# Optimization experiments

Hardware: AMD Instinct MI355X
Metric: run time of the kernel (lower is better)

Reference implementation:

```python
import jax, jax.numpy as jnp
import numpy as np

DIM = 128
CODEBOOK_SIZE = 1024

def setup_inputs() -> dict:
    key = jax.random.key(0)
    k1, k2 = jax.random.split(key)
    x = jax.random.normal(k1, (16, 4096, DIM), dtype=jnp.float32)
    embed = jax.random.normal(k2, (CODEBOOK_SIZE, DIM), dtype=jnp.float32)
    return {"x": x, "embed": embed}

def reference(x, embed):
    # preprocess: flatten leading dims -> (N, d)
    shape = x.shape
    flat = x.reshape(-1, shape[-1])  # (N, d)
    x_sq = jnp.sum(flat * flat, axis=1, keepdims=True)        # (N, 1)
    e_sq = jnp.sum(embed * embed, axis=1)[None, :]            # (1, K)
    dist = -(x_sq - 2.0 * (flat @ embed.T) + e_sq)            # (N, K)
    embed_ind = jnp.argmax(dist, axis=-1)                     # (N,)
    embed_ind = embed_ind.reshape(shape[:-1])                 # (...,)
    quantize = jnp.take(embed, embed_ind, axis=0)             # (..., d)
    return (quantize, embed_ind)
```

## Files before the change

### kernel.cpp

```cpp
#include <hip/hip_runtime.h>

#define NRD   65536
#define DIMD  128
#define KCB   1024
#define RPB   64
#define NBLK  (NRD / RPB)
#define MARGIN 0.10f

typedef float f32x4 __attribute__((ext_vector_type(4)));
typedef _Float16 half8 __attribute__((ext_vector_type(8)));

#define WS_ESQ   0
#define WS_CNT   4096
#define WS_LIST  8192
#define WS_B     270336
#define WS_ET2   532480
#define WS_NEED  1056768

__device__ inline half8 pack_h(float4 a, float4 b) {
    half8 r;
    r[0]=(_Float16)a.x; r[1]=(_Float16)a.y; r[2]=(_Float16)a.z; r[3]=(_Float16)a.w;
    r[4]=(_Float16)b.x; r[5]=(_Float16)b.y; r[6]=(_Float16)b.z; r[7]=(_Float16)b.w;
    return r;
}

__global__ __launch_bounds__(256, 2) void prep_kernel(const float* __restrict__ embed,
                                                      float* __restrict__ esq,
                                                      float4* __restrict__ bblob,
                                                      float4* __restrict__ et4,
                                                      int* __restrict__ cnt,
                                                      int doTrans) {
    __shared__ float tile[64][129];
    const int t = threadIdx.x;
    {
        int gw   = blockIdx.x * 4 + (t >> 6);
        int lane = t & 63;
        const float* row = embed + (size_t)gw * DIMD;
        float a = row[lane], b = row[lane + 64];
        float v = a * a + b * b;
        #pragma unroll
        for (int off = 32; off >= 1; off >>= 1) v += __shfl_xor(v, off, 64);
        if (lane == 0) esq[gw] = v;
    }
    if (blockIdx.x < 64) {
        int tid  = blockIdx.x * 256 + t;
        int lane = tid & 63;
        int ctg  = (tid >> 6) & 15;
        int ksh  = (tid >> 10) & 1;
        int s    = tid >> 11;
        int chunk = s >> 1, kh = s & 1;
        int ks = kh * 2 + ksh;
        int l15 = lane & 15, l4 = lane >> 4;
        int code = chunk * 256 + ctg * 16 + l15;
        int d0   = ks * 32 + l4 * 8;
        const float4* e4 = (const float4*)(embed + (size_t)code * DIMD + d0);
        half8 v = pack_h(e4[0], e4[1]);
        bblob[tid] = *(float4*)&v;
    }
    if (doTrans && blockIdx.x >= 64 && blockIdx.x < 80) {
        const int c0 = (blockIdx.x - 64) * 64;
        #pragma unroll
        for (int i = 0; i < 8; ++i) {
            int u = t + i * 256;
            int row = u >> 5, col4 = u & 31;
            float4 v = ((const float4*)embed)[(size_t)(c0 + row) * 32 + col4];
            tile[row][col4 * 4 + 0] = v.x;
            tile[row][col4 * 4 + 1] = v.y;
            tile[row][col4 * 4 + 2] = v.z;
            tile[row][col4 * 4 + 3] = v.w;
        }
        __syncthreads();
        #pragma unroll
        for (int i = 0; i < 8; ++i) {
            int u = t + i * 256;
            int d = u >> 4, off = u & 15;
            float4 v;
            v.x = tile[off * 4 + 0][d];
            v.y = tile[off * 4 + 1][d];
            v.z = tile[off * 4 + 2][d];
            v.w = tile[off * 4 + 3][d];
            et4[(size_t)d * 256 + (c0 >> 2) + off] = v;
        }
    }
    if (blockIdx.x == 128 && t == 0) cnt[0] = 0;
}

__global__ __launch_bounds__(512, 4) void vq_mfma(const float* __restrict__ x,
                                                  const float* __restrict__ embed,
                                                  const float* __restrict__ esq,
                                                  const float4* __restrict__ bblob,
                                                  float* __restrict__ out_q,
                                                  float* __restrict__ out_idx,
                                                  int* __restrict__ cnt,
                                                  int* __restrict__ list) {
    __shared__ __align__(16) short Bb[32][512];
    __shared__ float rbest[4][RPB];
    __shared__ int   rmeta[4][RPB];
    __shared__ float rb2[4][RPB];

    const int t    = threadIdx.x;
    const int lane = t & 63;
    const int w    = __builtin_amdgcn_readfirstlane(t >> 6);
    const int rg   = w >> 2, cg = w & 3;
    const int l15  = lane & 15, l4 = lane >> 4;
    const int row0 = blockIdx.x * RPB;

    short (*Atrans)[4][512] = (short (*)[4][512])&Bb[0][0];

    const int ksA = w & 3, jh = w >> 2;
    const float4* xs = (const float4*)(x + (size_t)(row0 + lane) * DIMD + ksA * 32 + jh * 16);
    float4 xv0 = xs[0], xv1 = xs[1], xv2 = xs[2], xv3 = xs[3];

    const int rtA = lane >> 4, riA = lane & 15;
    *(half8*)&Atrans[ksA][rtA][((jh * 2 + 0) * 16 + riA) * 8] = pack_h(xv0, xv1);
    *(half8*)&Atrans[ksA][rtA][((jh * 2 + 1) * 16 + riA) * 8] = pack_h(xv2, xv3);
    asm volatile("s_waitcnt lgkmcnt(0)" ::: "memory");
    __builtin_amdgcn_s_barrier();

    half8 ahr[4][2];
    #pragma unroll
    for (int ks = 0; ks < 4; ++ks)
        #pragma unroll
        for (int rt = 0; rt < 2; ++rt)
            ahr[ks][rt] = *(const half8*)&Atrans[ks][rg * 2 + rt][lane * 8];
    asm volatile("s_waitcnt lgkmcnt(0)" ::: "memory");
    __builtin_amdgcn_s_barrier();

#define GLDS(sv) do {                                                                                   \
    const char* g_ = (const char*)bblob + (size_t)(sv) * 32768 + ((size_t)w * 64 + lane) * 16;          \
    _Pragma("unroll")                                                                                   \
    for (int k_ = 0; k_ < 4; ++k_)                                                                      \
        __builtin_amdgcn_global_load_lds(                                                               \
            (const __attribute__((address_space(1))) unsigned int*)(g_ + k_ * 8192),                    \
            (__attribute__((address_space(3))) unsigned int*)&Bb[k_ * 8 + w][0], 16, 0, 0);             \
} while (0)

    GLDS(0);
    asm volatile("s_waitcnt vmcnt(0)" ::: "memory");
    __builtin_amdgcn_s_barrier();

    f32x4 acc[2][4];
    float best[2][4]; int bidx[2][4]; float b2[2][4];
    #pragma unroll
    for (int i = 0; i < 2; ++i)
        #pragma unroll
        for (int j = 0; j < 4; ++j) { best[i][j] = -1e30f; bidx[i][j] = 0; b2[i][j] = -1e30f; }

    const float* esqp = esq + cg * 64 + l15;
    float eq0 = 0.f, eq1 = 0.f, eq2 = 0.f, eq3 = 0.f;

#define STEP(khv) do {                                                                  \
    const int s_ = c * 2 + khv;                                                         \
    if (khv == 0) {                                                                     \
        eq0 = esqp[c * 256];      eq1 = esqp[c * 256 + 16];                             \
        eq2 = esqp[c * 256 + 32]; eq3 = esqp[c * 256 + 48];                             \
        _Pragma("unroll")                                                               \
        for (int i_ = 0; i_ < 2; ++i_)                                                  \
            _Pragma("unroll")                                                           \
            for (int j_ = 0; j_ < 4; ++j_) acc[i_][j_] = (f32x4){0.f, 0.f, 0.f, 0.f};   \
    }                                                                                   \
    half8 bh_[2][4];                                                                    \
    _Pragma("unroll")                                                                   \
    for (int ksh_ = 0; ksh_ < 2; ++ksh_)                                                \
        _Pragma("unroll")                                                               \
        for (int ct_ = 0; ct_ < 4; ++ct_)                                               \
            bh_[ksh_][ct_] = *(const half8*)&Bb[ksh_ * 16 + cg * 4 + ct_][lane * 8];    \
    asm volatile("s_waitcnt lgkmcnt(0)" ::: "memory");                                  \
    __builtin_amdgcn_s_barrier();                            \
    if (s_ < 7) GLDS(s_ + 1);                                   \
    _Pragma("unroll")                                                                   \
    for (int ksh_ = 0; ksh_ < 2; ++ksh_) {                                              \
        _Pragma("unroll")                                                               \
        for (int ct_ = 0; ct_ < 4; ++ct_) {                                             \
            _Pragma("unroll")                                                           \
            for (int rt_ = 0; rt_ < 2; ++rt_)                                           \
                acc[rt_][ct_] = __builtin_amdgcn_mfma_f32_16x16x32_f16(ahr[khv * 2 + ksh_][rt_], bh_[ksh_][ct_], acc[rt_][ct_], 0, 0, 0); \
        }                                                                               \
    }                                                                                   \
    if (khv == 1) {                           \
        _Pragma("unroll")                                                               \
        for (int ct_ = 0; ct_ < 4; ++ct_) {                                             \
            int code_ = c * 256 + cg * 64 + ct_ * 16 + l15;                             \
            float eq_ = (ct_ == 0) ? eq0 : (ct_ == 1) ? eq1 : (ct_ == 2) ? eq2 : eq3;   \
            _Pragma("unroll")                                                           \
            for (int rt_ = 0; rt_ < 2; ++rt_)                                           \
                _Pragma("unroll")                                                       \
                for (int r_ = 0; r_ < 4; ++r_) {                                        \
                    float sc_ = 2.0f * acc[rt_][ct_][r_] - eq_;                         \
                    b2[rt_][r_] = fmaxf(b2[rt_][r_], fminf(sc_, best[rt_][r_]));        \
                    if (sc_ > best[rt_][r_]) { best[rt_][r_] = sc_; bidx[rt_][r_] = code_; } \
                }                                                                       \
        }                                                                               \
    }                                                                                   \
    if (s_ < 7) {                                                                       \
        asm volatile("s_waitcnt vmcnt(0)" ::: "memory");          \
        __builtin_amdgcn_s_barrier();                                                   \
    }                                                                                   \
} while (0)

    for (int c = 0; c < 4; ++c) {
        STEP(0); STEP(1);
    }
#undef STEP
#undef GLDS

    #pragma unroll
    for (int rt = 0; rt < 2; ++rt)
        #pragma unroll
        for (int r = 0; r < 4; ++r) {
            float v = best[rt][r]; int i = bidx[rt][r]; float s2 = b2[rt][r];
            #pragma unroll
            for (int off = 1; off < 16; off <<= 1) {
                float ov = __shfl_xor(v, off, 64);
                int   oi = __shfl_xor(i, off, 64);
                float o2 = __shfl_xor(s2, off, 64);
                s2 = fmaxf(fmaxf(s2, o2), fminf(v, ov));
                bool sw = (ov > v) || (ov == v && oi < i);
                if (sw) { v = ov; i = oi; }
            }
            if (l15 == 0) {
                int rl = rg * 32 + rt * 16 + l4 * 4 + r;
                rbest[cg][rl] = v;
                rmeta[cg][rl] = i;
                rb2[cg][rl]   = s2;
            }
        }
    __syncthreads();
    if (t < RPB) {
        float b = rbest[0][t]; int i = rmeta[0][t]; float s2 = rb2[0][t];
        #pragma unroll
        for (int g = 1; g < 4; ++g) {
            float ob = rbest[g][t]; int oi = rmeta[g][t]; float o2 = rb2[g][t];
            s2 = fmaxf(fmaxf(s2, o2), fminf(b, ob));
            bool sw = (ob > b) || (ob == b && oi < i);
            if (sw) { b = ob; i = oi; }
        }
        out_idx[row0 + t] = (float)i;
        if (s2 >= b - MARGIN) { int pos = atomicAdd(cnt, 1); list[pos] = row0 + t; }
        rmeta[0][t] = i;
    }
    __syncthreads();
    {
        int row = t >> 3, part = t & 7;
        int idx = rmeta[0][row];
        const float4* src = (const float4*)(embed + (size_t)idx * DIMD + part * 16);
        float4* dst = (float4*)(out_q + (size_t)(row0 + row) * DIMD + part * 16);
        #pragma unroll
        for (int q = 0; q < 4; ++q) dst[q] = src[q];
    }
}

__global__ __launch_bounds__(256, 2) void trans_kernel(const float* __restrict__ embed,
                                                       float4* __restrict__ et4) {
    __shared__ float tile[64][129];
    const int t = threadIdx.x;
    const int c0 = blockIdx.x * 64;
    #pragma unroll
    for (int i = 0; i < 8; ++i) {
        int u = t + i * 256;
        int row = u >> 5, col4 = u & 31;
        float4 v = ((const float4*)embed)[(size_t)(c0 + row) * 32 + col4];
        tile[row][col4 * 4 + 0] = v.x;
        tile[row][col4 * 4 + 1] = v.y;
        tile[row][col4 * 4 + 2] = v.z;
        tile[row][col4 * 4 + 3] = v.w;
    }
    __syncthreads();
    #pragma unroll
    for (int i = 0; i < 8; ++i) {
        int u = t + i * 256;
        int d = u >> 4, off = u & 15;
        float4 v;
        v.x = tile[off * 4 + 0][d];
        v.y = tile[off * 4 + 1][d];
        v.z = tile[off * 4 + 2][d];
        v.w = tile[off * 4 + 3][d];
        et4[(size_t)d * 256 + (c0 >> 2) + off] = v;
    }
}

__global__ __launch_bounds__(256, 2) void refine_kernel(const float* __restrict__ x,
                                                        const float* __restrict__ embed,
                                                        const float* __restrict__ esq,
                                                        const f32x4* __restrict__ et4,
                                                        float* __restrict__ out_q,
                                                        float* __restrict__ out_idx,
                                                        const int* __restrict__ cnt,
                                                        const int* __restrict__ list) {
    __shared__ float xls[4][4][128];
    const int t = threadIdx.x, lane = t & 63, w = t >> 6;
    const int n = cnt[0];
    const int njobs = (n + 3) >> 2;
    for (int job = blockIdx.x * 4 + w; job < njobs; job += gridDim.x * 4) {
        int rows[4];
        #pragma unroll
        for (int i = 0; i < 4; ++i) {
            int li = job * 4 + i; if (li >= n) li = n - 1;
            rows[i] = list[li];
        }
        float xsq[4];
        #pragma unroll
        for (int i = 0; i < 4; ++i) {
            float2 xv = *(const float2*)(x + (size_t)rows[i] * DIMD + lane * 2);
            xls[w][i][lane * 2]     = xv.x;
            xls[w][i][lane * 2 + 1] = xv.y;
            float s = xv.x * xv.x + xv.y * xv.y;
            #pragma unroll
            for (int off = 32; off >= 1; off >>= 1) s += __shfl_xor(s, off, 64);
            xsq[i] = s;
        }
        f32x4 acc[4][4];
        #pragma unroll
        for (int i = 0; i < 4; ++i)
            #pragma unroll
            for (int g = 0; g < 4; ++g) acc[i][g] = (f32x4){0.f, 0.f, 0.f, 0.f};

        for (int d0 = 0; d0 < 32; ++d0) {
            float4 xd[4];
            #pragma unroll
            for (int i = 0; i < 4; ++i) xd[i] = *(const float4*)&xls[w][i][d0 * 4];
            #pragma unroll
            for (int dd = 0; dd < 4; ++dd) {
                const f32x4* ep = et4 + (size_t)(d0 * 4 + dd) * 256 + lane;
                f32x4 e0 = ep[0], e1 = ep[64], e2 = ep[128], e3 = ep[192];
                #pragma unroll
                for (int i = 0; i < 4; ++i) {
                    float xsc = (dd == 0) ? xd[i].x : (dd == 1) ? xd[i].y
                              : (dd == 2) ? xd[i].z : xd[i].w;
                    acc[i][0] = e0 * xsc + acc[i][0];
                    acc[i][1] = e1 * xsc + acc[i][1];
                    acc[i][2] = e2 * xsc + acc[i][2];
                    acc[i][3] = e3 * xsc + acc[i][3];
                }
            }
        }

        #pragma unroll
        for (int i = 0; i < 4; ++i) {
            float bv = -1e30f; int bi = 0;
            #pragma unroll
            for (int g = 0; g < 4; ++g) {
                float4 eq = *(const float4*)&esq[g * 256 + lane * 4];
                #pragma unroll
                for (int c2 = 0; c2 < 4; ++c2) {
                    float eqv = (c2 == 0) ? eq.x : (c2 == 1) ? eq.y : (c2 == 2) ? eq.z : eq.w;
                    float sc = -(__fadd_rn(__fsub_rn(xsq[i], __fmul_rn(2.0f, acc[i][g][c2])), eqv));
                    int code = g * 256 + lane * 4 + c2;
                    if (sc > bv) { bv = sc; bi = code; }
                }
            }
            #pragma unroll
            for (int off = 32; off >= 1; off >>= 1) {
                float ov = __shfl_xor(bv, off, 64);
                int   oi = __shfl_xor(bi, off, 64);
                if (ov > bv || (ov == bv && oi < bi)) { bv = ov; bi = oi; }
            }
            if (lane == 0) out_idx[rows[i]] = (float)bi;
            if (lane < 32) {
                float4 v = ((const float4*)embed)[(size_t)bi * 32 + lane];
                ((float4*)out_q)[(size_t)rows[i] * 32 + lane] = v;
            }
        }
    }
}

extern "C" void kernel_launch(void* const* d_in, const int* in_sizes, int n_in,
                              void* d_out, int out_size, void* d_ws, size_t ws_size,
                              hipStream_t stream) {
    const float* x     = (const float*)d_in[0];
    const float* embed = (const float*)d_in[1];
    float* out     = (float*)d_out;
    float* out_q   = out;
    float* out_idx = out + (size_t)NRD * DIMD;

    char*  wsb  = (char*)d_ws;
    float* esq  = (float*)(wsb + WS_ESQ);
    int*   cnt  = (int*)(wsb + WS_CNT);
    int*   list = (int*)(wsb + WS_LIST);
    float4* bblob = (float4*)(wsb + WS_B);

    const int fused = (ws_size >= (size_t)WS_NEED) ? 1 : 0;
    f32x4* et4 = fused ? (f32x4*)(wsb + WS_ET2) : (f32x4*)(wsb + WS_B);

    prep_kernel  <<<dim3(256),  dim3(256), 0, stream>>>(embed, esq, bblob, (float4*)et4, cnt, fused);
    vq_mfma      <<<dim3(NBLK), dim3(512), 0, stream>>>(x, embed, esq, bblob, out_q, out_idx, cnt, list);
    if (!fused)
        trans_kernel<<<dim3(16), dim3(256), 0, stream>>>(embed, (float4*)et4);
    refine_kernel<<<dim3(512),  dim3(256), 0, stream>>>(x, embed, esq, et4, out_q, out_idx, cnt, list);
}
```

Before: 79.28 us.

## Double rows per block and halve codebook stage width in VQ MFMA kernel

Each block now handles 128 rows instead of 64. Its 8 waves are split as 4 row groups by 2 code groups, and the codebook is streamed in 16 stages of 128 codes rather than 8 stages of 256, with the B blob relaid out to match. A separate LDS buffer for the A tile lets the first codebook stage load overlap with the A register reads. Each streamed codebook tile is now reused across twice as many rows, halving the B traffic per row, at the cost of more barrier stages and fewer blocks. The refine launch grid is also halved.

```diff
diff --git a/kernel.cpp b/kernel.cpp
--- a/kernel.cpp
+++ b/kernel.cpp
@@ -3,7 +3,7 @@
 #define NRD   65536
 #define DIMD  128
 #define KCB   1024
-#define RPB   64
+#define RPB   128
 #define NBLK  (NRD / RPB)
 #define MARGIN 0.10f
 
@@ -43,16 +43,15 @@
         if (lane == 0) esq[gw] = v;
     }
     if (blockIdx.x < 64) {
-        int tid  = blockIdx.x * 256 + t;
-        int lane = tid & 63;
-        int ctg  = (tid >> 6) & 15;
-        int ksh  = (tid >> 10) & 1;
-        int s    = tid >> 11;
-        int chunk = s >> 1, kh = s & 1;
-        int ks = kh * 2 + ksh;
-        int l15 = lane & 15, l4 = lane >> 4;
-        int code = chunk * 256 + ctg * 16 + l15;
-        int d0   = ks * 32 + l4 * 8;
+        int tid = blockIdx.x * 256 + t;
+        int ci  = tid & 15;
+        int k8  = (tid >> 4) & 3;
+        int ctg = (tid >> 6) & 7;
+        int ksl = (tid >> 9) & 1;
+        int s2  = tid >> 10;
+        int c   = s2 >> 1, kh = s2 & 1;
+        int code = c * 128 + ctg * 16 + ci;
+        int d0   = kh * 64 + ksl * 32 + k8 * 8;
         const float4* e4 = (const float4*)(embed + (size_t)code * DIMD + d0);
         half8 v = pack_h(e4[0], e4[1]);
         bblob[tid] = *(float4*)&v;
@@ -93,50 +92,51 @@
                                                   float* __restrict__ out_idx,
                                                   int* __restrict__ cnt,
                                                   int* __restrict__ list) {
-    __shared__ __align__(16) short Bb[32][512];
-    __shared__ float rbest[4][RPB];
-    __shared__ int   rmeta[4][RPB];
-    __shared__ float rb2[4][RPB];
+    __shared__ __align__(16) short Atrans[4][8][512];
+    __shared__ __align__(16) short Bb[16][512];
+    __shared__ float rbest[2][RPB];
+    __shared__ int   rmeta[2][RPB];
+    __shared__ float rb2[2][RPB];
 
     const int t    = threadIdx.x;
     const int lane = t & 63;
     const int w    = __builtin_amdgcn_readfirstlane(t >> 6);
-    const int rg   = w >> 2, cg = w & 3;
+    const int rg   = w >> 1;
+    const int cg   = w & 1;
     const int l15  = lane & 15, l4 = lane >> 4;
     const int row0 = blockIdx.x * RPB;
 
-    short (*Atrans)[4][512] = (short (*)[4][512])&Bb[0][0];
-
-    const int ksA = w & 3, jh = w >> 2;
-    const float4* xs = (const float4*)(x + (size_t)(row0 + lane) * DIMD + ksA * 32 + jh * 16);
-    float4 xv0 = xs[0], xv1 = xs[1], xv2 = xs[2], xv3 = xs[3];
-
-    const int rtA = lane >> 4, riA = lane & 15;
-    *(half8*)&Atrans[ksA][rtA][((jh * 2 + 0) * 16 + riA) * 8] = pack_h(xv0, xv1);
-    *(half8*)&Atrans[ksA][rtA][((jh * 2 + 1) * 16 + riA) * 8] = pack_h(xv2, xv3);
+    const int rh = w >> 2, ksA = w & 3;
+    const float4* xs = (const float4*)(x + (size_t)(row0 + rh * 64 + lane) * DIMD + ksA * 32);
+    float4 xv[8];
+    #pragma unroll
+    for (int q = 0; q < 8; ++q) xv[q] = xs[q];
+
+    const int rtg = rh * 4 + (lane >> 4), ri = lane & 15;
+    #pragma unroll
+    for (int k8 = 0; k8 < 4; ++k8)
+        *(half8*)&Atrans[ksA][rtg][(k8 * 16 + ri) * 8] = pack_h(xv[2 * k8], xv[2 * k8 + 1]);
     asm volatile("s_waitcnt lgkmcnt(0)" ::: "memory");
     __builtin_amdgcn_s_barrier();
 
-    half8 ahr[4][2];
-    #pragma unroll
-    for (int ks = 0; ks < 4; ++ks)
-        #pragma unroll
-        for (int rt = 0; rt < 2; ++rt)
-            ahr[ks][rt] = *(const half8*)&Atrans[ks][rg * 2 + rt][lane * 8];
-    asm volatile("s_waitcnt lgkmcnt(0)" ::: "memory");
-    __builtin_amdgcn_s_barrier();
-
 #define GLDS(sv) do {                                                                                   \
-    const char* g_ = (const char*)bblob + (size_t)(sv) * 32768 + ((size_t)w * 64 + lane) * 16;          \
+    const char* g_ = (const char*)bblob + (size_t)(sv) * 16384 + ((size_t)w * 64 + lane) * 16;          \
     _Pragma("unroll")                                                                                   \
-    for (int k_ = 0; k_ < 4; ++k_)                                                                      \
+    for (int k_ = 0; k_ < 2; ++k_)                                                                      \
         __builtin_amdgcn_global_load_lds(                                                               \
             (const __attribute__((address_space(1))) unsigned int*)(g_ + k_ * 8192),                    \
             (__attribute__((address_space(3))) unsigned int*)&Bb[k_ * 8 + w][0], 16, 0, 0);             \
 } while (0)
 
     GLDS(0);
-    asm volatile("s_waitcnt vmcnt(0)" ::: "memory");
+
+    half8 ahr[4][2];
+    #pragma unroll
+    for (int ks = 0; ks < 4; ++ks)
+        #pragma unroll
+        for (int rt = 0; rt < 2; ++rt)
+            ahr[ks][rt] = *(const half8*)&Atrans[ks][rg * 2 + rt][lane * 8];
+    asm volatile("s_waitcnt vmcnt(0) lgkmcnt(0)" ::: "memory");
     __builtin_amdgcn_s_barrier();
 
     f32x4 acc[2][4];
@@ -149,11 +149,11 @@
     const float* esqp = esq + cg * 64 + l15;
     float eq0 = 0.f, eq1 = 0.f, eq2 = 0.f, eq3 = 0.f;
 
-#define STEP(khv) do {                                                                  \
-    const int s_ = c * 2 + khv;                                                         \
-    if (khv == 0) {                                                                     \
-        eq0 = esqp[c * 256];      eq1 = esqp[c * 256 + 16];                             \
-        eq2 = esqp[c * 256 + 32]; eq3 = esqp[c * 256 + 48];                             \
+#define STEP(kh) do {                                                                   \
+    const int s_ = c * 2 + kh;                                                          \
+    if (kh == 0) {                                                                      \
+        eq0 = esqp[c * 128];      eq1 = esqp[c * 128 + 16];                             \
+        eq2 = esqp[c * 128 + 32]; eq3 = esqp[c * 128 + 48];                             \
         _Pragma("unroll")                                                               \
         for (int i_ = 0; i_ < 2; ++i_)                                                  \
             _Pragma("unroll")                                                           \
@@ -161,26 +161,26 @@
     }                                                                                   \
     half8 bh_[2][4];                                                                    \
     _Pragma("unroll")                                                                   \
-    for (int ksh_ = 0; ksh_ < 2; ++ksh_)                                                \
+    for (int ksl_ = 0; ksl_ < 2; ++ksl_)                                                \
         _Pragma("unroll")                                                               \
         for (int ct_ = 0; ct_ < 4; ++ct_)                                               \
-            bh_[ksh_][ct_] = *(const half8*)&Bb[ksh_ * 16 + cg * 4 + ct_][lane * 8];    \
+            bh_[ksl_][ct_] = *(const half8*)&Bb[ksl_ * 8 + cg * 4 + ct_][lane * 8];     \
     asm volatile("s_waitcnt lgkmcnt(0)" ::: "memory");                                  \
     __builtin_amdgcn_s_barrier();                            \
-    if (s_ < 7) GLDS(s_ + 1);                                   \
+    if (s_ < 15) GLDS(s_ + 1);                                  \
     _Pragma("unroll")                                                                   \
-    for (int ksh_ = 0; ksh_ < 2; ++ksh_) {                                              \
+    for (int ksl_ = 0; ksl_ < 2; ++ksl_) {                                              \
         _Pragma("unroll")                                                               \
         for (int ct_ = 0; ct_ < 4; ++ct_) {                                             \
             _Pragma("unroll")                                                           \
             for (int rt_ = 0; rt_ < 2; ++rt_)                                           \
-                acc[rt_][ct_] = __builtin_amdgcn_mfma_f32_16x16x32_f16(ahr[khv * 2 + ksh_][rt_], bh_[ksh_][ct_], acc[rt_][ct_], 0, 0, 0); \
+                acc[rt_][ct_] = __builtin_amdgcn_mfma_f32_16x16x32_f16(ahr[kh * 2 + ksl_][rt_], bh_[ksl_][ct_], acc[rt_][ct_], 0, 0, 0); \
         }                                                                               \
     }                                                                                   \
-    if (khv == 1) {                           \
+    if (kh == 1) {                            \
         _Pragma("unroll")                                                               \
         for (int ct_ = 0; ct_ < 4; ++ct_) {                                             \
-            int code_ = c * 256 + cg * 64 + ct_ * 16 + l15;                             \
+            int code_ = c * 128 + cg * 64 + ct_ * 16 + l15;                             \
             float eq_ = (ct_ == 0) ? eq0 : (ct_ == 1) ? eq1 : (ct_ == 2) ? eq2 : eq3;   \
             _Pragma("unroll")                                                           \
             for (int rt_ = 0; rt_ < 2; ++rt_)                                           \
@@ -192,13 +192,13 @@
                 }                                                                       \
         }                                                                               \
     }                                                                                   \
-    if (s_ < 7) {                                                                       \
+    if (s_ < 15) {                                                                      \
         asm volatile("s_waitcnt vmcnt(0)" ::: "memory");          \
         __builtin_amdgcn_s_barrier();                                                   \
     }                                                                                   \
 } while (0)
 
-    for (int c = 0; c < 4; ++c) {
+    for (int c = 0; c < 8; ++c) {
         STEP(0); STEP(1);
     }
 #undef STEP
@@ -228,9 +228,8 @@
     __syncthreads();
     if (t < RPB) {
         float b = rbest[0][t]; int i = rmeta[0][t]; float s2 = rb2[0][t];
-        #pragma unroll
-        for (int g = 1; g < 4; ++g) {
-            float ob = rbest[g][t]; int oi = rmeta[g][t]; float o2 = rb2[g][t];
+        {
+            float ob = rbest[1][t]; int oi = rmeta[1][t]; float o2 = rb2[1][t];
             s2 = fmaxf(fmaxf(s2, o2), fminf(b, ob));
             bool sw = (ob > b) || (ob == b && oi < i);
             if (sw) { b = ob; i = oi; }
@@ -241,12 +240,12 @@
     }
     __syncthreads();
     {
-        int row = t >> 3, part = t & 7;
+        int row = t >> 2, part = t & 3;
         int idx = rmeta[0][row];
-        const float4* src = (const float4*)(embed + (size_t)idx * DIMD + part * 16);
-        float4* dst = (float4*)(out_q + (size_t)(row0 + row) * DIMD + part * 16);
-        #pragma unroll
-        for (int q = 0; q < 4; ++q) dst[q] = src[q];
+        const float4* src = (const float4*)(embed + (size_t)idx * DIMD + part * 32);
+        float4* dst = (float4*)(out_q + (size_t)(row0 + row) * DIMD + part * 32);
+        #pragma unroll
+        for (int q = 0; q < 8; ++q) dst[q] = src[q];
     }
 }
 
@@ -386,5 +385,5 @@
     vq_mfma      <<<dim3(NBLK), dim3(512), 0, stream>>>(x, embed, esq, bblob, out_q, out_idx, cnt, list);
     if (!fused)
         trans_kernel<<<dim3(16), dim3(256), 0, stream>>>(embed, (float4*)et4);
-    refine_kernel<<<dim3(512),  dim3(256), 0, stream>>>(x, embed, esq, et4, out_q, out_idx, cnt, list);
-}
+    refine_kernel<<<dim3(256),  dim3(256), 0, stream>>>(x, embed, esq, et4, out_q, out_idx, cnt, list);
+}
```

New measurement: 81.97 us. 1.03x slower.
